# Kernel tuning notes

Hardware: AMD Instinct MI355X
Metric: run time of the kernel (lower is better)

The kernel has to match this reference:

```python
import jax, jax.numpy as jnp
import numpy as np

B, L, D_IN, D_H = 8, 16384, 256, 256  # leaves L = 2**14, complete binary tree
N = 2 * L - 1  # total nodes, heap layout: children of j are 2j+1, 2j+2


def setup_inputs() -> dict:
    key = jax.random.key(0)
    ks = jax.random.split(key, 7)
    s_in = 1.0 / float(np.sqrt(D_IN))
    s_h = 1.0 / float(np.sqrt(D_H))
    return {
        "x": jax.random.normal(ks[0], (B, N, D_IN), jnp.float32),
        "W_iou": jax.random.uniform(ks[1], (D_IN, 3 * D_H), jnp.float32, -s_in, s_in),
        "b_iou": jax.random.uniform(ks[2], (3 * D_H,), jnp.float32, -s_in, s_in),
        "U_iou": jax.random.uniform(ks[3], (D_H, 3 * D_H), jnp.float32, -s_h, s_h),
        "W_f": jax.random.uniform(ks[4], (D_IN, D_H), jnp.float32, -s_in, s_in),
        "b_f": jax.random.uniform(ks[5], (D_IN,)[:0] + (D_H,), jnp.float32, -s_in, s_in),
        "U_f": jax.random.uniform(ks[6], (D_H, D_H), jnp.float32, -s_h, s_h),
    }


def reference(x, W_iou, b_iou, U_iou, W_f, b_f, U_f):
    Bn, Nn, _ = x.shape
    H = U_f.shape[0]
    Lv = (Nn + 1) // 2  # number of leaves
    depth = int(np.log2(Lv))

    # --- leaf nodes (no children): heap indices Lv-1 .. 2Lv-2 ---
    x_leaf = x[:, Lv - 1:, :]                       # [B, L, d_in]
    iou = x_leaf @ W_iou + b_iou                    # [B, L, 3H]
    i, o, u = jnp.split(iou, 3, axis=-1)
    c = jax.nn.sigmoid(i) * jnp.tanh(u)
    h = jax.nn.sigmoid(o) * jnp.tanh(c)             # [B, L, H]

    # --- internal levels, bottom-up; each node has exactly 2 children ---
    n = Lv
    for _ in range(depth):
        n //= 2
        x_lvl = x[:, n - 1:2 * n - 1, :]            # [B, n, d_in]
        hc = h.reshape(Bn, n, 2, H)                 # children hidden states
        cc = c.reshape(Bn, n, 2, H)                 # children cell states
        h_sum = hc.sum(axis=2)                      # child-sum  [B, n, H]
        iou = x_lvl @ W_iou + b_iou + h_sum @ U_iou
        i, o, u = jnp.split(iou, 3, axis=-1)
        # per-child forget gate: sigmoid(W_f x + b_f + U_f h_j)
        f = jax.nn.sigmoid((x_lvl @ W_f + b_f)[:, :, None, :]
                           + jnp.einsum('bnch,hk->bnck', hc, U_f))
        c = jax.nn.sigmoid(i) * jnp.tanh(u) + (f * cc).sum(axis=2)
        h = jax.nn.sigmoid(o) * jnp.tanh(c)

    # root h, c concatenated -> [B, 2H]
    return jnp.concatenate([h[:, 0, :], c[:, 0, :]], axis=-1)
```

## Files before the change

kernel.cpp:

```cpp
#include <hip/hip_runtime.h>
#include <math.h>


#define Bb 8
#define Lleaf 16384
#define Nn 32767
#define NInt 16383
#define Dd 256

typedef __attribute__((ext_vector_type(8))) short short8;
typedef __attribute__((ext_vector_type(4))) float float4v;

__device__ __forceinline__ float sigf(float x) {
    return __builtin_amdgcn_rcpf(1.0f + __expf(-x));
}
__device__ __forceinline__ float tanh_fast(float x) {
    return fmaf(2.0f, sigf(2.0f * x), -1.0f);
}
__device__ __forceinline__ unsigned short f2bf(float f) {
    unsigned int u = __float_as_uint(f);
    u = (u + 0x7FFFu + ((u >> 16) & 1u)) >> 16;
    return (unsigned short)u;
}
__device__ __forceinline__ float bf2f(unsigned short h) {
    return __uint_as_float(((unsigned int)h) << 16);
}
__device__ __forceinline__ void load_lds16(const void* g, void* l) {
    __builtin_amdgcn_global_load_lds(
        (const __attribute__((address_space(1))) unsigned int*)g,
        (__attribute__((address_space(3))) unsigned int*)l, 16, 0, 0);
}

__global__ __launch_bounds__(256) void xcast(
    const float* __restrict__ x, unsigned short* __restrict__ xbf)
{
    const int base = (blockIdx.x * 256 + threadIdx.x) * 8;
    const int node = base >> 8;
    const int b = node / NInt, g = node - b * NInt;
    const int off = base & 255;
    const float4* p = (const float4*)(x + (((size_t)(b * Nn + g)) << 8) + off);
    const float4 f0 = p[0], f1 = p[1];
    union { unsigned short us[8]; uint4 v; } pk;
    pk.us[0] = f2bf(f0.x); pk.us[1] = f2bf(f0.y);
    pk.us[2] = f2bf(f0.z); pk.us[3] = f2bf(f0.w);
    pk.us[4] = f2bf(f1.x); pk.us[5] = f2bf(f1.y);
    pk.us[6] = f2bf(f1.z); pk.us[7] = f2bf(f1.w);
    *(uint4*)(xbf + base) = pk.v;
}

__global__ __launch_bounds__(256) void pack_internal(
    const float* __restrict__ W_iou, const float* __restrict__ U_iou,
    const float* __restrict__ W_f,   const float* __restrict__ U_f,
    unsigned short* __restrict__ Bt)
{
    const int idx = blockIdx.x * 256 + threadIdx.x;
    const int col = idx / 768, k = idx - col * 768;
    const int q = col / 80, rem = col - q * 80;
    const int g = rem >> 4, r = rem & 15;
    const int d = (q << 4) + r;
    const int seg = k >> 8, kk = k & 255;
    float val;
    if (g < 3) {
        val = (seg == 0) ? W_iou[kk * 768 + g * 256 + d]
                         : U_iou[kk * 768 + g * 256 + d];
    } else if (seg == 0) {
        val = W_f[kk * 256 + d];
    } else if (seg == 1) {
        val = (g == 3) ? U_f[kk * 256 + d] : 0.0f;
    } else {
        val = (g == 4) ? U_f[kk * 256 + d] : 0.0f;
    }
    Bt[idx] = f2bf(val);
}

__global__ __launch_bounds__(256) void pack_leaf(
    const float* __restrict__ W_iou, unsigned short* __restrict__ Btl)
{
    const int idx = blockIdx.x * 256 + threadIdx.x;
    const int col = idx >> 8, k = idx & 255;
    const int q = col / 48, rem = col - q * 48;
    const int g = rem >> 4, r = rem & 15;
    const int d = (q << 4) + r;
    Btl[idx] = f2bf(W_iou[k * 768 + g * 256 + d]);
}

__global__ __launch_bounds__(256, 3) void gemm_level_big(
    const unsigned short* __restrict__ xbf, const unsigned short* __restrict__ Bt,
    const float* __restrict__ b_iou, const float* __restrict__ b_f,
    unsigned short* __restrict__ hbuf, float* __restrict__ cbuf,
    int n, int lvl)
{
    __shared__ unsigned short Alds[128 * 64];
    __shared__ unsigned short Blds[160 * 64];
    const int tid  = threadIdx.x;
    const int wave = tid >> 6, lane = tid & 63;
    const int l16  = lane & 15, q4 = lane >> 4;
    const int m0   = blockIdx.x * 128;
    const int n0   = blockIdx.y * 160;
    const int lr   = lane >> 3;
    const int lp   = (lane & 7) ^ lr;

    const int b  = m0 >> lvl;
    const int j0 = m0 & (n - 1);
    const int xb0 = b * NInt + n - 1 + j0;
    const int cb0 = b * Nn + 2 * n - 1 + 2 * j0;
    const int ob0 = b * Nn + n - 1 + j0;

    float4v acc[2][10];
    #pragma unroll
    for (int qq = 0; qq < 2; ++qq) {
        const int d = ((blockIdx.y * 2 + qq) << 4) + l16;
        float bv0 = b_iou[d], bv1 = b_iou[256 + d], bv2 = b_iou[512 + d];
        float bv3 = b_f[d];
        float bv[5] = {bv0, bv1, bv2, bv3, bv3};
        #pragma unroll
        for (int g = 0; g < 5; ++g) {
            float4v v; v[0] = bv[g]; v[1] = bv[g]; v[2] = bv[g]; v[3] = bv[g];
            acc[0][qq * 5 + g] = v; acc[1][qq * 5 + g] = v;
        }
    }

    for (int kk = 0; kk < 12; ++kk) {
        __syncthreads();
        #pragma unroll
        for (int it = 0; it < 4; ++it) {
            const int g = it * 4 + wave;
            const int r = g * 8 + lr;
            const unsigned short* src;
            if (kk < 4) {
                src = xbf + (((xb0 + r) << 8) + kk * 64 + lp * 8);
            } else {
                const int sel = (kk >= 8) ? 1 : 0;
                src = hbuf + (((cb0 + 2 * r + sel) << 8) + ((kk - 4) & 3) * 64 + lp * 8);
            }
            load_lds16(src, &Alds[g * 512]);
        }
        #pragma unroll
        for (int it = 0; it < 5; ++it) {
            const int g = it * 4 + wave;
            const int row = g * 8 + lr;
            load_lds16(Bt + ((n0 + row) * 768 + kk * 64 + lp * 8), &Blds[g * 512]);
        }
        __syncthreads();
        #pragma unroll
        for (int ks = 0; ks < 2; ++ks) {
            const int pa = ks * 4 + q4;
            const int sw = (pa ^ (l16 & 7)) * 8;
            const short8 a0 = *(const short8*)&Alds[(wave * 32 + l16) * 64 + sw];
            const short8 a1 = *(const short8*)&Alds[(wave * 32 + 16 + l16) * 64 + sw];
            #pragma unroll
            for (int ni = 0; ni < 10; ++ni) {
                const short8 bf = *(const short8*)&Blds[(ni * 16 + l16) * 64 + sw];
                acc[0][ni] = __builtin_amdgcn_mfma_f32_16x16x32_bf16(a0, bf, acc[0][ni], 0, 0, 0);
                acc[1][ni] = __builtin_amdgcn_mfma_f32_16x16x32_bf16(a1, bf, acc[1][ni], 0, 0, 0);
            }
        }
    }

    #pragma unroll
    for (int mi = 0; mi < 2; ++mi) {
        #pragma unroll
        for (int reg = 0; reg < 4; ++reg) {
            const int row_l = wave * 32 + mi * 16 + (q4 << 2) + reg;
            const int cbase = (cb0 + 2 * row_l) << 8;
            const int obase = (ob0 + row_l) << 8;
            #pragma unroll
            for (int qq = 0; qq < 2; ++qq) {
                const int d = ((blockIdx.y * 2 + qq) << 4) + l16;
                const float i_ = acc[mi][qq * 5 + 0][reg];
                const float o_ = acc[mi][qq * 5 + 1][reg];
                const float u_ = acc[mi][qq * 5 + 2][reg];
                const float f1 = acc[mi][qq * 5 + 3][reg];
                const float f2 = acc[mi][qq * 5 + 4][reg];
                const float c1 = cbuf[cbase + d];
                const float c2 = cbuf[cbase + 256 + d];
                const float c = sigf(i_) * tanh_fast(u_) + sigf(f1) * c1 + sigf(f2) * c2;
                const float h = sigf(o_) * tanh_fast(c);
                cbuf[obase + d] = c;
                hbuf[obase + d] = f2bf(h);
            }
        }
    }
}

__global__ __launch_bounds__(256) void gemm_level(
    const unsigned short* __restrict__ xbf, const unsigned short* __restrict__ Bt,
    const float* __restrict__ b_iou, const float* __restrict__ b_f,
    unsigned short* __restrict__ hbuf, float* __restrict__ cbuf,
    int n, int lvl)
{
    __shared__ unsigned short Alds[128 * 64];
    __shared__ unsigned short Blds[160 * 64];
    const int tid  = threadIdx.x;
    const int wave = tid >> 6, lane = tid & 63;
    const int l16  = lane & 15, q4 = lane >> 4;
    const int m0   = blockIdx.x * 128;
    const int n0   = blockIdx.y * 160;
    const int lr   = lane >> 3;
    const int lp   = (lane & 7) ^ lr;

    float4v acc[2][10];
    #pragma unroll
    for (int qq = 0; qq < 2; ++qq) {
        const int d = ((blockIdx.y * 2 + qq) << 4) + l16;
        float bv0 = b_iou[d], bv1 = b_iou[256 + d], bv2 = b_iou[512 + d];
        float bv3 = b_f[d];
        float bv[5] = {bv0, bv1, bv2, bv3, bv3};
        #pragma unroll
        for (int g = 0; g < 5; ++g) {
            float4v v; v[0] = bv[g]; v[1] = bv[g]; v[2] = bv[g]; v[3] = bv[g];
            acc[0][qq * 5 + g] = v; acc[1][qq * 5 + g] = v;
        }
    }

    for (int kk = 0; kk < 12; ++kk) {
        __syncthreads();
        #pragma unroll
        for (int it = 0; it < 4; ++it) {
            const int g = it * 4 + wave;
            const int r = g * 8 + lr;
            const int m = m0 + r;
            const int b = m >> lvl, j = m & (n - 1);
            const unsigned short* src;
            if (kk < 4) {
                src = xbf + (((b * NInt + n - 1 + j) << 8) + kk * 64 + lp * 8);
            } else {
                const int child = 2 * n - 1 + 2 * j + (kk >= 8 ? 1 : 0);
                src = hbuf + (((b * Nn + child) << 8) + ((kk - 4) & 3) * 64 + lp * 8);
            }
            load_lds16(src, &Alds[g * 512]);
        }
        #pragma unroll
        for (int it = 0; it < 5; ++it) {
            const int g = it * 4 + wave;
            const int row = g * 8 + lr;
            load_lds16(Bt + ((n0 + row) * 768 + kk * 64 + lp * 8), &Blds[g * 512]);
        }
        __syncthreads();
        #pragma unroll
        for (int ks = 0; ks < 2; ++ks) {
            const int pa = ks * 4 + q4;
            const int sw = (pa ^ (l16 & 7)) * 8;
            const short8 a0 = *(const short8*)&Alds[(wave * 32 + l16) * 64 + sw];
            const short8 a1 = *(const short8*)&Alds[(wave * 32 + 16 + l16) * 64 + sw];
            #pragma unroll
            for (int ni = 0; ni < 10; ++ni) {
                const short8 bf = *(const short8*)&Blds[(ni * 16 + l16) * 64 + sw];
                acc[0][ni] = __builtin_amdgcn_mfma_f32_16x16x32_bf16(a0, bf, acc[0][ni], 0, 0, 0);
                acc[1][ni] = __builtin_amdgcn_mfma_f32_16x16x32_bf16(a1, bf, acc[1][ni], 0, 0, 0);
            }
        }
    }

    #pragma unroll
    for (int mi = 0; mi < 2; ++mi) {
        #pragma unroll
        for (int reg = 0; reg < 4; ++reg) {
            const int row_l = wave * 32 + mi * 16 + (q4 << 2) + reg;
            const int m = m0 + row_l;
            const int b = m >> lvl, j = m & (n - 1);
            const int nb = b * Nn;
            const int cbase = (nb + 2 * n - 1 + 2 * j) << 8;
            const int obase = (nb + n - 1 + j) << 8;
            #pragma unroll
            for (int qq = 0; qq < 2; ++qq) {
                const int d = ((blockIdx.y * 2 + qq) << 4) + l16;
                const float i_ = acc[mi][qq * 5 + 0][reg];
                const float o_ = acc[mi][qq * 5 + 1][reg];
                const float u_ = acc[mi][qq * 5 + 2][reg];
                const float f1 = acc[mi][qq * 5 + 3][reg];
                const float f2 = acc[mi][qq * 5 + 4][reg];
                const float c1 = cbuf[cbase + d];
                const float c2 = cbuf[cbase + 256 + d];
                const float c = sigf(i_) * tanh_fast(u_) + sigf(f1) * c1 + sigf(f2) * c2;
                const float h = sigf(o_) * tanh_fast(c);
                cbuf[obase + d] = c;
                hbuf[obase + d] = f2bf(h);
            }
        }
    }
}

__global__ __launch_bounds__(256) void gemm_small(
    const unsigned short* __restrict__ xbf, const unsigned short* __restrict__ Bt,
    const float* __restrict__ b_iou, const float* __restrict__ b_f,
    unsigned short* __restrict__ hbuf, float* __restrict__ cbuf,
    int n, int lvl)
{
    __shared__ unsigned short Alds[64 * 64];
    __shared__ unsigned short Blds[160 * 64];
    const int tid  = threadIdx.x;
    const int wave = tid >> 6, lane = tid & 63;
    const int l16  = lane & 15, q4 = lane >> 4;
    const int n0   = blockIdx.y * 160;
    const int lr   = lane >> 3;
    const int lp   = (lane & 7) ^ lr;
    const int rmax = 8 * n - 1;

    float4v acc[10];
    #pragma unroll
    for (int qq = 0; qq < 2; ++qq) {
        const int d = ((blockIdx.y * 2 + qq) << 4) + l16;
        float bv0 = b_iou[d], bv1 = b_iou[256 + d], bv2 = b_iou[512 + d];
        float bv3 = b_f[d];
        float bv[5] = {bv0, bv1, bv2, bv3, bv3};
        #pragma unroll
        for (int g = 0; g < 5; ++g) {
            float4v v; v[0] = bv[g]; v[1] = bv[g]; v[2] = bv[g]; v[3] = bv[g];
            acc[qq * 5 + g] = v;
        }
    }

    for (int kk = 0; kk < 12; ++kk) {
        __syncthreads();
        #pragma unroll
        for (int it = 0; it < 2; ++it) {
            const int g = it * 4 + wave;
            const int r = g * 8 + lr;
            const int m = (r > rmax) ? rmax : r;
            const int b = m >> lvl, j = m & (n - 1);
            const unsigned short* src;
            if (kk < 4) {
                src = xbf + (((b * NInt + n - 1 + j) << 8) + kk * 64 + lp * 8);
            } else {
                const int child = 2 * n - 1 + 2 * j + (kk >= 8 ? 1 : 0);
                src = hbuf + (((b * Nn + child) << 8) + ((kk - 4) & 3) * 64 + lp * 8);
            }
            load_lds16(src, &Alds[g * 512]);
        }
        #pragma unroll
        for (int it = 0; it < 5; ++it) {
            const int g = it * 4 + wave;
            const int row = g * 8 + lr;
            load_lds16(Bt + ((n0 + row) * 768 + kk * 64 + lp * 8), &Blds[g * 512]);
        }
        __syncthreads();
        #pragma unroll
        for (int ks = 0; ks < 2; ++ks) {
            const int pa = ks * 4 + q4;
            const int sw = (pa ^ (l16 & 7)) * 8;
            const short8 a0 = *(const short8*)&Alds[(wave * 16 + l16) * 64 + sw];
            #pragma unroll
            for (int ni = 0; ni < 10; ++ni) {
                const short8 bf = *(const short8*)&Blds[(ni * 16 + l16) * 64 + sw];
                acc[ni] = __builtin_amdgcn_mfma_f32_16x16x32_bf16(a0, bf, acc[ni], 0, 0, 0);
            }
        }
    }

    #pragma unroll
    for (int reg = 0; reg < 4; ++reg) {
        const int row_l = wave * 16 + (q4 << 2) + reg;
        const int m = (row_l > rmax) ? rmax : row_l;
        const bool valid = (row_l <= rmax);
        const int b = m >> lvl, j = m & (n - 1);
        const int nb = b * Nn;
        const int cbase = (nb + 2 * n - 1 + 2 * j) << 8;
        const int obase = (nb + n - 1 + j) << 8;
        #pragma unroll
        for (int qq = 0; qq < 2; ++qq) {
            const int d = ((blockIdx.y * 2 + qq) << 4) + l16;
            const float i_ = acc[qq * 5 + 0][reg];
            const float o_ = acc[qq * 5 + 1][reg];
            const float u_ = acc[qq * 5 + 2][reg];
            const float f1 = acc[qq * 5 + 3][reg];
            const float f2 = acc[qq * 5 + 4][reg];
            const float c1 = cbuf[cbase + d];
            const float c2 = cbuf[cbase + 256 + d];
            const float c = sigf(i_) * tanh_fast(u_) + sigf(f1) * c1 + sigf(f2) * c2;
            const float h = sigf(o_) * tanh_fast(c);
            if (valid) {
                cbuf[obase + d] = c;
                hbuf[obase + d] = f2bf(h);
            }
        }
    }
}

__global__ __launch_bounds__(256, 3) void gemm_leaf(
    const float* __restrict__ x, const unsigned short* __restrict__ Btl,
    const float* __restrict__ b_iou,
    unsigned short* __restrict__ hbuf, float* __restrict__ cbuf)
{
    __shared__ unsigned short Alds[128 * 64];
    __shared__ unsigned short Blds[96 * 64];
    const int tid  = threadIdx.x;
    const int wave = tid >> 6, lane = tid & 63;
    const int l16  = lane & 15, q4 = lane >> 4;
    const int m0   = blockIdx.x * 128;
    const int n0   = blockIdx.y * 96;
    const int lr   = lane >> 3;
    const int lp   = (lane & 7) ^ lr;

    const int b   = m0 >> 14;
    const int j0  = m0 & (Lleaf - 1);
    const int nb0 = b * Nn + (Lleaf - 1) + j0;

    float4v acc[2][6];
    #pragma unroll
    for (int qq = 0; qq < 2; ++qq) {
        const int d = ((blockIdx.y * 2 + qq) << 4) + l16;
        float bv[3] = {b_iou[d], b_iou[256 + d], b_iou[512 + d]};
        #pragma unroll
        for (int g = 0; g < 3; ++g) {
            float4v v; v[0] = bv[g]; v[1] = bv[g]; v[2] = bv[g]; v[3] = bv[g];
            acc[0][qq * 3 + g] = v; acc[1][qq * 3 + g] = v;
        }
    }

    for (int kk = 0; kk < 4; ++kk) {
        __syncthreads();
        {
            int task = tid;
            #pragma unroll
            for (int it = 0; it < 4; ++it, task += 256) {
                const int r = task >> 3, k8 = task & 7;
                const float4* p = (const float4*)(x +
                    (((nb0 + r) << 8) + kk * 64 + (k8 << 3)));
                const float4 f0 = p[0], f1 = p[1];
                union { unsigned short us[8]; uint4 v; } pk;
                pk.us[0] = f2bf(f0.x); pk.us[1] = f2bf(f0.y);
                pk.us[2] = f2bf(f0.z); pk.us[3] = f2bf(f0.w);
                pk.us[4] = f2bf(f1.x); pk.us[5] = f2bf(f1.y);
                pk.us[6] = f2bf(f1.z); pk.us[7] = f2bf(f1.w);
                *(uint4*)&Alds[(r * 8 + (k8 ^ (r & 7))) * 8] = pk.v;
            }
        }
        #pragma unroll
        for (int it = 0; it < 3; ++it) {
            const int g = it * 4 + wave;
            const int row = g * 8 + lr;
            load_lds16(Btl + ((n0 + row) * 256 + kk * 64 + lp * 8), &Blds[g * 512]);
        }
        __syncthreads();
        #pragma unroll
        for (int ks = 0; ks < 2; ++ks) {
            const int pa = ks * 4 + q4;
            const int sw = (pa ^ (l16 & 7)) * 8;
            const short8 a0 = *(const short8*)&Alds[(wave * 32 + l16) * 64 + sw];
            const short8 a1 = *(const short8*)&Alds[(wave * 32 + 16 + l16) * 64 + sw];
            #pragma unroll
            for (int ni = 0; ni < 6; ++ni) {
                const short8 bf = *(const short8*)&Blds[(ni * 16 + l16) * 64 + sw];
                acc[0][ni] = __builtin_amdgcn_mfma_f32_16x16x32_bf16(a0, bf, acc[0][ni], 0, 0, 0);
                acc[1][ni] = __builtin_amdgcn_mfma_f32_16x16x32_bf16(a1, bf, acc[1][ni], 0, 0, 0);
            }
        }
    }

    #pragma unroll
    for (int mi = 0; mi < 2; ++mi) {
        #pragma unroll
        for (int reg = 0; reg < 4; ++reg) {
            const int row_l = wave * 32 + mi * 16 + (q4 << 2) + reg;
            const int obase = (nb0 + row_l) << 8;
            #pragma unroll
            for (int qq = 0; qq < 2; ++qq) {
                const int d = ((blockIdx.y * 2 + qq) << 4) + l16;
                const float i_ = acc[mi][qq * 3 + 0][reg];
                const float o_ = acc[mi][qq * 3 + 1][reg];
                const float u_ = acc[mi][qq * 3 + 2][reg];
                const float c = sigf(i_) * tanh_fast(u_);
                const float h = sigf(o_) * tanh_fast(c);
                cbuf[obase + d] = c;
                hbuf[obase + d] = f2bf(h);
            }
        }
    }
}

__global__ __launch_bounds__(256) void out_kernel(
    const unsigned short* __restrict__ hbuf, const float* __restrict__ cbuf,
    float* __restrict__ out)
{
    const int t = threadIdx.x;
    const int b = blockIdx.x;
    out[b * 512 + t]       = bf2f(hbuf[(b * Nn) * Dd + t]);
    out[b * 512 + 256 + t] = cbuf[(b * Nn) * Dd + t];
}

extern "C" void kernel_launch(void* const* d_in, const int* in_sizes, int n_in,
                              void* d_out, int out_size, void* d_ws, size_t ws_size,
                              hipStream_t stream) {
    const float* x     = (const float*)d_in[0];
    const float* W_iou = (const float*)d_in[1];
    const float* b_iou = (const float*)d_in[2];
    const float* U_iou = (const float*)d_in[3];
    const float* W_f   = (const float*)d_in[4];
    const float* b_f   = (const float*)d_in[5];
    const float* U_f   = (const float*)d_in[6];
    float* out = (float*)d_out;

    const size_t HB = (size_t)Bb * Nn * Dd;
    unsigned short* hbuf = (unsigned short*)d_ws;
    float* cbuf = (float*)((char*)d_ws + HB * 2);
    unsigned short* xbf = (unsigned short*)((char*)d_ws + HB * 6);
    unsigned short* Bt  = xbf + (size_t)Bb * NInt * Dd;
    unsigned short* Btl = Bt + 1280 * 768;

    xcast<<<NInt, 256, 0, stream>>>(x, xbf);
    pack_internal<<<(1280 * 768) / 256, 256, 0, stream>>>(W_iou, U_iou, W_f, U_f, Bt);
    pack_leaf<<<(768 * 256) / 256, 256, 0, stream>>>(W_iou, Btl);

    gemm_leaf<<<dim3((Bb * Lleaf) / 128, 8), 256, 0, stream>>>(x, Btl, b_iou, hbuf, cbuf);

    for (int lvl = 13; lvl >= 7; --lvl) {
        const int n = 1 << lvl;
        gemm_level_big<<<dim3((Bb * n) / 128, 8), 256, 0, stream>>>(
            xbf, Bt, b_iou, b_f, hbuf, cbuf, n, lvl);
    }
    for (int lvl = 6; lvl >= 4; --lvl) {
        const int n = 1 << lvl;
        gemm_level<<<dim3((Bb * n) / 128, 8), 256, 0, stream>>>(
            xbf, Bt, b_iou, b_f, hbuf, cbuf, n, lvl);
    }
    for (int lvl = 3; lvl >= 0; --lvl) {
        const int n = 1 << lvl;
        gemm_small<<<dim3(1, 8), 256, 0, stream>>>(
            xbf, Bt, b_iou, b_f, hbuf, cbuf, n, lvl);
    }
    out_kernel<<<Bb, 256, 0, stream>>>(hbuf, cbuf, out);
}
```

Before: 1.050 ms.

## Use compact ping-pong h/c buffers per level and precast all of x to bf16

Replaces the heap-indexed h/c buffers with dense ping-pong buffers laid out per level by batch and node, so child and output rows are contiguous. The leaf GEMM now reads a bf16 copy of x made by xcast, which converts every node instead of only internal ones, and no longer casts fp32 inside the kernel. The big-level and leaf grids are flattened to 1D with the column-tile index in the low bits, so the eight column tiles of one row tile are scheduled together for A-tile reuse in L2. The goal is a smaller working set and simpler addressing, at the cost of a separate full-size cast pass over x.

```diff
diff --git a/kernel.cpp b/kernel.cpp
--- a/kernel.cpp
+++ b/kernel.cpp
@@ -5,7 +5,6 @@
 #define Bb 8
 #define Lleaf 16384
 #define Nn 32767
-#define NInt 16383
 #define Dd 256
 
 typedef __attribute__((ext_vector_type(8))) short short8;
@@ -35,10 +34,7 @@
     const float* __restrict__ x, unsigned short* __restrict__ xbf)
 {
     const int base = (blockIdx.x * 256 + threadIdx.x) * 8;
-    const int node = base >> 8;
-    const int b = node / NInt, g = node - b * NInt;
-    const int off = base & 255;
-    const float4* p = (const float4*)(x + (((size_t)(b * Nn + g)) << 8) + off);
+    const float4* p = (const float4*)(x + base);
     const float4 f0 = p[0], f1 = p[1];
     union { unsigned short us[8]; uint4 v; } pk;
     pk.us[0] = f2bf(f0.x); pk.us[1] = f2bf(f0.y);
@@ -87,7 +83,107 @@
 __global__ __launch_bounds__(256, 3) void gemm_level_big(
     const unsigned short* __restrict__ xbf, const unsigned short* __restrict__ Bt,
     const float* __restrict__ b_iou, const float* __restrict__ b_f,
-    unsigned short* __restrict__ hbuf, float* __restrict__ cbuf,
+    unsigned short* __restrict__ h_out, float* __restrict__ c_out,
+    const unsigned short* __restrict__ h_ch, const float* __restrict__ c_ch,
+    int n, int lvl)
+{
+    __shared__ unsigned short Alds[128 * 64];
+    __shared__ unsigned short Blds[160 * 64];
+    const int tid  = threadIdx.x;
+    const int wave = tid >> 6, lane = tid & 63;
+    const int l16  = lane & 15, q4 = lane >> 4;
+    const int bx   = blockIdx.x >> 3, by = blockIdx.x & 7;
+    const int m0   = bx * 128;
+    const int n0   = by * 160;
+    const int lr   = lane >> 3;
+    const int lp   = (lane & 7) ^ lr;
+
+    const int b   = m0 >> lvl;
+    const int xr0 = m0 + (n - 1) + b * (Nn - n);
+
+    float4v acc[2][10];
+    #pragma unroll
+    for (int qq = 0; qq < 2; ++qq) {
+        const int d = ((by * 2 + qq) << 4) + l16;
+        float bv0 = b_iou[d], bv1 = b_iou[256 + d], bv2 = b_iou[512 + d];
+        float bv3 = b_f[d];
+        float bv[5] = {bv0, bv1, bv2, bv3, bv3};
+        #pragma unroll
+        for (int g = 0; g < 5; ++g) {
+            float4v v; v[0] = bv[g]; v[1] = bv[g]; v[2] = bv[g]; v[3] = bv[g];
+            acc[0][qq * 5 + g] = v; acc[1][qq * 5 + g] = v;
+        }
+    }
+
+    for (int kk = 0; kk < 12; ++kk) {
+        __syncthreads();
+        #pragma unroll
+        for (int it = 0; it < 4; ++it) {
+            const int g = it * 4 + wave;
+            const int r = g * 8 + lr;
+            const unsigned short* src;
+            if (kk < 4) {
+                src = xbf + (((xr0 + r) << 8) + kk * 64 + lp * 8);
+            } else {
+                const int sel = (kk >= 8) ? 1 : 0;
+                src = h_ch + (((2 * (m0 + r) + sel) << 8) + ((kk - 4) & 3) * 64 + lp * 8);
+            }
+            load_lds16(src, &Alds[g * 512]);
+        }
+        #pragma unroll
+        for (int it = 0; it < 5; ++it) {
+            const int g = it * 4 + wave;
+            const int row = g * 8 + lr;
+            load_lds16(Bt + ((n0 + row) * 768 + kk * 64 + lp * 8), &Blds[g * 512]);
+        }
+        __syncthreads();
+        #pragma unroll
+        for (int ks = 0; ks < 2; ++ks) {
+            const int pa = ks * 4 + q4;
+            const int sw = (pa ^ (l16 & 7)) * 8;
+            const short8 a0 = *(const short8*)&Alds[(wave * 32 + l16) * 64 + sw];
+            const short8 a1 = *(const short8*)&Alds[(wave * 32 + 16 + l16) * 64 + sw];
+            #pragma unroll
+            for (int ni = 0; ni < 10; ++ni) {
+                const short8 bf = *(const short8*)&Blds[(ni * 16 + l16) * 64 + sw];
+                acc[0][ni] = __builtin_amdgcn_mfma_f32_16x16x32_bf16(a0, bf, acc[0][ni], 0, 0, 0);
+                acc[1][ni] = __builtin_amdgcn_mfma_f32_16x16x32_bf16(a1, bf, acc[1][ni], 0, 0, 0);
+            }
+        }
+    }
+
+    #pragma unroll
+    for (int mi = 0; mi < 2; ++mi) {
+        #pragma unroll
+        for (int reg = 0; reg < 4; ++reg) {
+            const int row_l = wave * 32 + mi * 16 + (q4 << 2) + reg;
+            const int m = m0 + row_l;
+            const int cbase = (2 * m) << 8;
+            const int obase = m << 8;
+            #pragma unroll
+            for (int qq = 0; qq < 2; ++qq) {
+                const int d = ((by * 2 + qq) << 4) + l16;
+                const float i_ = acc[mi][qq * 5 + 0][reg];
+                const float o_ = acc[mi][qq * 5 + 1][reg];
+                const float u_ = acc[mi][qq * 5 + 2][reg];
+                const float f1 = acc[mi][qq * 5 + 3][reg];
+                const float f2 = acc[mi][qq * 5 + 4][reg];
+                const float c1 = c_ch[cbase + d];
+                const float c2 = c_ch[cbase + 256 + d];
+                const float c = sigf(i_) * tanh_fast(u_) + sigf(f1) * c1 + sigf(f2) * c2;
+                const float h = sigf(o_) * tanh_fast(c);
+                c_out[obase + d] = c;
+                h_out[obase + d] = f2bf(h);
+            }
+        }
+    }
+}
+
+__global__ __launch_bounds__(256) void gemm_level(
+    const unsigned short* __restrict__ xbf, const unsigned short* __restrict__ Bt,
+    const float* __restrict__ b_iou, const float* __restrict__ b_f,
+    unsigned short* __restrict__ h_out, float* __restrict__ c_out,
+    const unsigned short* __restrict__ h_ch, const float* __restrict__ c_ch,
     int n, int lvl)
 {
     __shared__ unsigned short Alds[128 * 64];
@@ -100,12 +196,6 @@
     const int lr   = lane >> 3;
     const int lp   = (lane & 7) ^ lr;
 
-    const int b  = m0 >> lvl;
-    const int j0 = m0 & (n - 1);
-    const int xb0 = b * NInt + n - 1 + j0;
-    const int cb0 = b * Nn + 2 * n - 1 + 2 * j0;
-    const int ob0 = b * Nn + n - 1 + j0;
-
     float4v acc[2][10];
     #pragma unroll
     for (int qq = 0; qq < 2; ++qq) {
@@ -126,12 +216,14 @@
         for (int it = 0; it < 4; ++it) {
             const int g = it * 4 + wave;
             const int r = g * 8 + lr;
+            const int m = m0 + r;
             const unsigned short* src;
             if (kk < 4) {
-                src = xbf + (((xb0 + r) << 8) + kk * 64 + lp * 8);
+                const int b = m >> lvl;
+                src = xbf + (((m + (n - 1) + b * (Nn - n)) << 8) + kk * 64 + lp * 8);
             } else {
                 const int sel = (kk >= 8) ? 1 : 0;
-                src = hbuf + (((cb0 + 2 * r + sel) << 8) + ((kk - 4) & 3) * 64 + lp * 8);
+                src = h_ch + (((2 * m + sel) << 8) + ((kk - 4) & 3) * 64 + lp * 8);
             }
             load_lds16(src, &Alds[g * 512]);
         }
@@ -162,8 +254,9 @@
         #pragma unroll
         for (int reg = 0; reg < 4; ++reg) {
             const int row_l = wave * 32 + mi * 16 + (q4 << 2) + reg;
-            const int cbase = (cb0 + 2 * row_l) << 8;
-            const int obase = (ob0 + row_l) << 8;
+            const int m = m0 + row_l;
+            const int cbase = (2 * m) << 8;
+            const int obase = m << 8;
             #pragma unroll
             for (int qq = 0; qq < 2; ++qq) {
                 const int d = ((blockIdx.y * 2 + qq) << 4) + l16;
@@ -172,110 +265,12 @@
                 const float u_ = acc[mi][qq * 5 + 2][reg];
                 const float f1 = acc[mi][qq * 5 + 3][reg];
                 const float f2 = acc[mi][qq * 5 + 4][reg];
-                const float c1 = cbuf[cbase + d];
-                const float c2 = cbuf[cbase + 256 + d];
+                const float c1 = c_ch[cbase + d];
+                const float c2 = c_ch[cbase + 256 + d];
                 const float c = sigf(i_) * tanh_fast(u_) + sigf(f1) * c1 + sigf(f2) * c2;
                 const float h = sigf(o_) * tanh_fast(c);
-                cbuf[obase + d] = c;
-                hbuf[obase + d] = f2bf(h);
-            }
-        }
-    }
-}
-
-__global__ __launch_bounds__(256) void gemm_level(
-    const unsigned short* __restrict__ xbf, const unsigned short* __restrict__ Bt,
-    const float* __restrict__ b_iou, const float* __restrict__ b_f,
-    unsigned short* __restrict__ hbuf, float* __restrict__ cbuf,
-    int n, int lvl)
-{
-    __shared__ unsigned short Alds[128 * 64];
-    __shared__ unsigned short Blds[160 * 64];
-    const int tid  = threadIdx.x;
-    const int wave = tid >> 6, lane = tid & 63;
-    const int l16  = lane & 15, q4 = lane >> 4;
-    const int m0   = blockIdx.x * 128;
-    const int n0   = blockIdx.y * 160;
-    const int lr   = lane >> 3;
-    const int lp   = (lane & 7) ^ lr;
-
-    float4v acc[2][10];
-    #pragma unroll
-    for (int qq = 0; qq < 2; ++qq) {
-        const int d = ((blockIdx.y * 2 + qq) << 4) + l16;
-        float bv0 = b_iou[d], bv1 = b_iou[256 + d], bv2 = b_iou[512 + d];
-        float bv3 = b_f[d];
-        float bv[5] = {bv0, bv1, bv2, bv3, bv3};
-        #pragma unroll
-        for (int g = 0; g < 5; ++g) {
-            float4v v; v[0] = bv[g]; v[1] = bv[g]; v[2] = bv[g]; v[3] = bv[g];
-            acc[0][qq * 5 + g] = v; acc[1][qq * 5 + g] = v;
-        }
-    }
-
-    for (int kk = 0; kk < 12; ++kk) {
-        __syncthreads();
-        #pragma unroll
-        for (int it = 0; it < 4; ++it) {
-            const int g = it * 4 + wave;
-            const int r = g * 8 + lr;
-            const int m = m0 + r;
-            const int b = m >> lvl, j = m & (n - 1);
-            const unsigned short* src;
-            if (kk < 4) {
-                src = xbf + (((b * NInt + n - 1 + j) << 8) + kk * 64 + lp * 8);
-            } else {
-                const int child = 2 * n - 1 + 2 * j + (kk >= 8 ? 1 : 0);
-                src = hbuf + (((b * Nn + child) << 8) + ((kk - 4) & 3) * 64 + lp * 8);
-            }
-            load_lds16(src, &Alds[g * 512]);
-        }
-        #pragma unroll
-        for (int it = 0; it < 5; ++it) {
-            const int g = it * 4 + wave;
-            const int row = g * 8 + lr;
-            load_lds16(Bt + ((n0 + row) * 768 + kk * 64 + lp * 8), &Blds[g * 512]);
-        }
-        __syncthreads();
-        #pragma unroll
-        for (int ks = 0; ks < 2; ++ks) {
-            const int pa = ks * 4 + q4;
-            const int sw = (pa ^ (l16 & 7)) * 8;
-            const short8 a0 = *(const short8*)&Alds[(wave * 32 + l16) * 64 + sw];
-            const short8 a1 = *(const short8*)&Alds[(wave * 32 + 16 + l16) * 64 + sw];
-            #pragma unroll
-            for (int ni = 0; ni < 10; ++ni) {
-                const short8 bf = *(const short8*)&Blds[(ni * 16 + l16) * 64 + sw];
-                acc[0][ni] = __builtin_amdgcn_mfma_f32_16x16x32_bf16(a0, bf, acc[0][ni], 0, 0, 0);
-                acc[1][ni] = __builtin_amdgcn_mfma_f32_16x16x32_bf16(a1, bf, acc[1][ni], 0, 0, 0);
-            }
-        }
-    }
-
-    #pragma unroll
-    for (int mi = 0; mi < 2; ++mi) {
-        #pragma unroll
-        for (int reg = 0; reg < 4; ++reg) {
-            const int row_l = wave * 32 + mi * 16 + (q4 << 2) + reg;
-            const int m = m0 + row_l;
-            const int b = m >> lvl, j = m & (n - 1);
-            const int nb = b * Nn;
-            const int cbase = (nb + 2 * n - 1 + 2 * j) << 8;
-            const int obase = (nb + n - 1 + j) << 8;
-            #pragma unroll
-            for (int qq = 0; qq < 2; ++qq) {
-                const int d = ((blockIdx.y * 2 + qq) << 4) + l16;
-                const float i_ = acc[mi][qq * 5 + 0][reg];
-                const float o_ = acc[mi][qq * 5 + 1][reg];
-                const float u_ = acc[mi][qq * 5 + 2][reg];
-                const float f1 = acc[mi][qq * 5 + 3][reg];
-                const float f2 = acc[mi][qq * 5 + 4][reg];
-                const float c1 = cbuf[cbase + d];
-                const float c2 = cbuf[cbase + 256 + d];
-                const float c = sigf(i_) * tanh_fast(u_) + sigf(f1) * c1 + sigf(f2) * c2;
-                const float h = sigf(o_) * tanh_fast(c);
-                cbuf[obase + d] = c;
-                hbuf[obase + d] = f2bf(h);
+                c_out[obase + d] = c;
+                h_out[obase + d] = f2bf(h);
             }
         }
     }
@@ -284,7 +279,8 @@
 __global__ __launch_bounds__(256) void gemm_small(
     const unsigned short* __restrict__ xbf, const unsigned short* __restrict__ Bt,
     const float* __restrict__ b_iou, const float* __restrict__ b_f,
-    unsigned short* __restrict__ hbuf, float* __restrict__ cbuf,
+    unsigned short* __restrict__ h_out, float* __restrict__ c_out,
+    const unsigned short* __restrict__ h_ch, const float* __restrict__ c_ch,
     int n, int lvl)
 {
     __shared__ unsigned short Alds[64 * 64];
@@ -318,13 +314,13 @@
             const int g = it * 4 + wave;
             const int r = g * 8 + lr;
             const int m = (r > rmax) ? rmax : r;
-            const int b = m >> lvl, j = m & (n - 1);
             const unsigned short* src;
             if (kk < 4) {
-                src = xbf + (((b * NInt + n - 1 + j) << 8) + kk * 64 + lp * 8);
+                const int b = m >> lvl;
+                src = xbf + (((m + (n - 1) + b * (Nn - n)) << 8) + kk * 64 + lp * 8);
             } else {
-                const int child = 2 * n - 1 + 2 * j + (kk >= 8 ? 1 : 0);
-                src = hbuf + (((b * Nn + child) << 8) + ((kk - 4) & 3) * 64 + lp * 8);
+                const int sel = (kk >= 8) ? 1 : 0;
+                src = h_ch + (((2 * m + sel) << 8) + ((kk - 4) & 3) * 64 + lp * 8);
             }
             load_lds16(src, &Alds[g * 512]);
         }
@@ -353,10 +349,8 @@
         const int row_l = wave * 16 + (q4 << 2) + reg;
         const int m = (row_l > rmax) ? rmax : row_l;
         const bool valid = (row_l <= rmax);
-        const int b = m >> lvl, j = m & (n - 1);
-        const int nb = b * Nn;
-        const int cbase = (nb + 2 * n - 1 + 2 * j) << 8;
-        const int obase = (nb + n - 1 + j) << 8;
+        const int cbase = (2 * m) << 8;
+        const int obase = m << 8;
         #pragma unroll
         for (int qq = 0; qq < 2; ++qq) {
             const int d = ((blockIdx.y * 2 + qq) << 4) + l16;
@@ -365,41 +359,41 @@
             const float u_ = acc[qq * 5 + 2][reg];
             const float f1 = acc[qq * 5 + 3][reg];
             const float f2 = acc[qq * 5 + 4][reg];
-            const float c1 = cbuf[cbase + d];
-            const float c2 = cbuf[cbase + 256 + d];
+            const float c1 = c_ch[cbase + d];
+            const float c2 = c_ch[cbase + 256 + d];
             const float c = sigf(i_) * tanh_fast(u_) + sigf(f1) * c1 + sigf(f2) * c2;
             const float h = sigf(o_) * tanh_fast(c);
             if (valid) {
-                cbuf[obase + d] = c;
-                hbuf[obase + d] = f2bf(h);
+                c_out[obase + d] = c;
+                h_out[obase + d] = f2bf(h);
             }
         }
     }
 }
 
 __global__ __launch_bounds__(256, 3) void gemm_leaf(
-    const float* __restrict__ x, const unsigned short* __restrict__ Btl,
+    const unsigned short* __restrict__ xbf, const unsigned short* __restrict__ Btl,
     const float* __restrict__ b_iou,
-    unsigned short* __restrict__ hbuf, float* __restrict__ cbuf)
+    unsigned short* __restrict__ h_out, float* __restrict__ c_out)
 {
     __shared__ unsigned short Alds[128 * 64];
     __shared__ unsigned short Blds[96 * 64];
     const int tid  = threadIdx.x;
     const int wave = tid >> 6, lane = tid & 63;
     const int l16  = lane & 15, q4 = lane >> 4;
-    const int m0   = blockIdx.x * 128;
-    const int n0   = blockIdx.y * 96;
+    const int bx   = blockIdx.x >> 3, by = blockIdx.x & 7;
+    const int m0   = bx * 128;
+    const int n0   = by * 96;
     const int lr   = lane >> 3;
     const int lp   = (lane & 7) ^ lr;
 
     const int b   = m0 >> 14;
-    const int j0  = m0 & (Lleaf - 1);
-    const int nb0 = b * Nn + (Lleaf - 1) + j0;
+    const int xr0 = m0 + (Lleaf - 1) + b * (Nn - Lleaf);
 
     float4v acc[2][6];
     #pragma unroll
     for (int qq = 0; qq < 2; ++qq) {
-        const int d = ((blockIdx.y * 2 + qq) << 4) + l16;
+        const int d = ((by * 2 + qq) << 4) + l16;
         float bv[3] = {b_iou[d], b_iou[256 + d], b_iou[512 + d]};
         #pragma unroll
         for (int g = 0; g < 3; ++g) {
@@ -410,21 +404,11 @@
 
     for (int kk = 0; kk < 4; ++kk) {
         __syncthreads();
-        {
-            int task = tid;
-            #pragma unroll
-            for (int it = 0; it < 4; ++it, task += 256) {
-                const int r = task >> 3, k8 = task & 7;
-                const float4* p = (const float4*)(x +
-                    (((nb0 + r) << 8) + kk * 64 + (k8 << 3)));
-                const float4 f0 = p[0], f1 = p[1];
-                union { unsigned short us[8]; uint4 v; } pk;
-                pk.us[0] = f2bf(f0.x); pk.us[1] = f2bf(f0.y);
-                pk.us[2] = f2bf(f0.z); pk.us[3] = f2bf(f0.w);
-                pk.us[4] = f2bf(f1.x); pk.us[5] = f2bf(f1.y);
-                pk.us[6] = f2bf(f1.z); pk.us[7] = f2bf(f1.w);
-                *(uint4*)&Alds[(r * 8 + (k8 ^ (r & 7))) * 8] = pk.v;
-            }
+        #pragma unroll
+        for (int it = 0; it < 4; ++it) {
+            const int g = it * 4 + wave;
+            const int r = g * 8 + lr;
+            load_lds16(xbf + (((xr0 + r) << 8) + kk * 64 + lp * 8), &Alds[g * 512]);
         }
         #pragma unroll
         for (int it = 0; it < 3; ++it) {
@@ -453,30 +437,30 @@
         #pragma unroll
         for (int reg = 0; reg < 4; ++reg) {
             const int row_l = wave * 32 + mi * 16 + (q4 << 2) + reg;
-            const int obase = (nb0 + row_l) << 8;
+            const int obase = (m0 + row_l) << 8;
             #pragma unroll
             for (int qq = 0; qq < 2; ++qq) {
-                const int d = ((blockIdx.y * 2 + qq) << 4) + l16;
+                const int d = ((by * 2 + qq) << 4) + l16;
                 const float i_ = acc[mi][qq * 3 + 0][reg];
                 const float o_ = acc[mi][qq * 3 + 1][reg];
                 const float u_ = acc[mi][qq * 3 + 2][reg];
                 const float c = sigf(i_) * tanh_fast(u_);
                 const float h = sigf(o_) * tanh_fast(c);
-                cbuf[obase + d] = c;
-                hbuf[obase + d] = f2bf(h);
+                c_out[obase + d] = c;
+                h_out[obase + d] = f2bf(h);
             }
         }
     }
 }
 
 __global__ __launch_bounds__(256) void out_kernel(
-    const unsigned short* __restrict__ hbuf, const float* __restrict__ cbuf,
+    const unsigned short* __restrict__ h_root, const float* __restrict__ c_root,
     float* __restrict__ out)
 {
     const int t = threadIdx.x;
     const int b = blockIdx.x;
-    out[b * 512 + t]       = bf2f(hbuf[(b * Nn) * Dd + t]);
-    out[b * 512 + 256 + t] = cbuf[(b * Nn) * Dd + t];
+    out[b * 512 + t]       = bf2f(h_root[(b << 8) + t]);
+    out[b * 512 + 256 + t] = c_root[(b << 8) + t];
 }
 
 extern "C" void kernel_launch(void* const* d_in, const int* in_sizes, int n_in,
@@ -491,33 +475,41 @@
     const float* U_f   = (const float*)d_in[6];
     float* out = (float*)d_out;
 
-    const size_t HB = (size_t)Bb * Nn * Dd;
-    unsigned short* hbuf = (unsigned short*)d_ws;
-    float* cbuf = (float*)((char*)d_ws + HB * 2);
-    unsigned short* xbf = (unsigned short*)((char*)d_ws + HB * 6);
-    unsigned short* Bt  = xbf + (size_t)Bb * NInt * Dd;
-    unsigned short* Btl = Bt + 1280 * 768;
-
-    xcast<<<NInt, 256, 0, stream>>>(x, xbf);
+    char* p = (char*)d_ws;
+    unsigned short* xbf = (unsigned short*)p;  p += (size_t)Bb * Nn * Dd * 2;
+    float* cE = (float*)p;                     p += (size_t)Bb * Lleaf * Dd * 4;
+    float* cO = (float*)p;                     p += (size_t)Bb * (Lleaf/2) * Dd * 4;
+    unsigned short* hE = (unsigned short*)p;   p += (size_t)Bb * Lleaf * Dd * 2;
+    unsigned short* hO = (unsigned short*)p;   p += (size_t)Bb * (Lleaf/2) * Dd * 2;
+    unsigned short* Bt  = (unsigned short*)p;  p += 1280 * 768 * 2;
+    unsigned short* Btl = (unsigned short*)p;
+
+    xcast<<<(Bb * Nn * Dd) / (256 * 8), 256, 0, stream>>>(x, xbf);
     pack_internal<<<(1280 * 768) / 256, 256, 0, stream>>>(W_iou, U_iou, W_f, U_f, Bt);
     pack_leaf<<<(768 * 256) / 256, 256, 0, stream>>>(W_iou, Btl);
 
-    gemm_leaf<<<dim3((Bb * Lleaf) / 128, 8), 256, 0, stream>>>(x, Btl, b_iou, hbuf, cbuf);
+    gemm_leaf<<<(Bb * Lleaf / 128) * 8, 256, 0, stream>>>(xbf, Btl, b_iou, hE, cE);
 
     for (int lvl = 13; lvl >= 7; --lvl) {
         const int n = 1 << lvl;
-        gemm_level_big<<<dim3((Bb * n) / 128, 8), 256, 0, stream>>>(
-            xbf, Bt, b_iou, b_f, hbuf, cbuf, n, lvl);
+        unsigned short* ho = (lvl & 1) ? hO : hE;  float* co = (lvl & 1) ? cO : cE;
+        unsigned short* hc = (lvl & 1) ? hE : hO;  float* cc = (lvl & 1) ? cE : cO;
+        gemm_level_big<<<(Bb * n / 128) * 8, 256, 0, stream>>>(
+            xbf, Bt, b_iou, b_f, ho, co, hc, cc, n, lvl);
     }
     for (int lvl = 6; lvl >= 4; --lvl) {
         const int n = 1 << lvl;
-        gemm_level<<<dim3((Bb * n) / 128, 8), 256, 0, stream>>>(
-            xbf, Bt, b_iou, b_f, hbuf, cbuf, n, lvl);
+        unsigned short* ho = (lvl & 1) ? hO : hE;  float* co = (lvl & 1) ? cO : cE;
+        unsigned short* hc = (lvl & 1) ? hE : hO;  float* cc = (lvl & 1) ? cE : cO;
+        gemm_level<<<dim3(Bb * n / 128, 8), 256, 0, stream>>>(
+            xbf, Bt, b_iou, b_f, ho, co, hc, cc, n, lvl);
     }
     for (int lvl = 3; lvl >= 0; --lvl) {
         const int n = 1 << lvl;
+        unsigned short* ho = (lvl & 1) ? hO : hE;  float* co = (lvl & 1) ? cO : cE;
+        unsigned short* hc = (lvl & 1) ? hE : hO;  float* cc = (lvl & 1) ? cE : cO;
         gemm_small<<<dim3(1, 8), 256, 0, stream>>>(
-            xbf, Bt, b_iou, b_f, hbuf, cbuf, n, lvl);
-    }
-    out_kernel<<<Bb, 256, 0, stream>>>(hbuf, cbuf, out);
-}
+            xbf, Bt, b_iou, b_f, ho, co, hc, cc, n, lvl);
+    }
+    out_kernel<<<Bb, 256, 0, stream>>>(hE, cE, out);
+}
```

New measurement: 981.5 us. 6.5% less time.
